# Performance work log

Hardware: AMD Instinct MI355X
Metric: run time of the kernel (lower is better)

The kernel has to match this reference:

```python
import jax, jax.numpy as jnp
import numpy as np

B, T, C, H = 4, 2048, 1024, 16
D = C // H  # key_dim = 64


def setup_inputs() -> dict:
    key = jax.random.key(0)
    k1, k2, k3 = jax.random.split(key, 3)
    x = jax.random.normal(k1, (B, T, C), dtype=jnp.float32)
    w_attn = jax.random.normal(k2, (C, 3 * C), dtype=jnp.float32) * 0.02
    b_attn = jnp.zeros((3 * C,), dtype=jnp.float32)
    w_proj = jax.random.normal(k3, (C, C), dtype=jnp.float32) * 0.02
    b_proj = jnp.zeros((C,), dtype=jnp.float32)
    return {"x": x, "w_attn": w_attn, "b_attn": b_attn,
            "w_proj": w_proj, "b_proj": b_proj}


def reference(x, w_attn, b_attn, w_proj, b_proj):
    b, t, c = x.shape
    d = c // H
    qkv = jnp.einsum('btc,cf->btf', x, w_attn) + b_attn  # [B,T,3C]
    q, k, v = jnp.split(qkv, 3, axis=-1)
    # [B,T,C] -> [B,H,T,D]
    q = q.reshape(b, t, H, d).transpose(0, 2, 1, 3)
    k = k.reshape(b, t, H, d).transpose(0, 2, 1, 3)
    v = v.reshape(b, t, H, d).transpose(0, 2, 1, 3)
    att = jnp.einsum('bhqd,bhkd->bhqk', q, k) / jnp.sqrt(jnp.float32(d))
    att = jax.nn.softmax(att, axis=-1)  # non-causal, full attention
    # dropout layers are identity at inference (rate=0.0 config)
    y = jnp.einsum('bhqk,bhkd->bhqd', att, v)
    y = y.transpose(0, 2, 1, 3).reshape(b, t, c)
    return jnp.einsum('btc,cf->btf', y, w_proj) + b_proj
```

## Files before the change

### kernel.cpp

```cpp
#include <hip/hip_runtime.h>
#include <math.h>

#define BB 4
#define TT 2048
#define CC 1024
#define HH 16
#define F3 3072
#define NTOK (BB*TT)
#define KDIM 1024

typedef __attribute__((ext_vector_type(8))) short short8;
typedef __attribute__((ext_vector_type(8))) unsigned short ushort8;
typedef __attribute__((ext_vector_type(8))) _Float16 half8;
typedef __attribute__((ext_vector_type(4))) unsigned short ushort4v;
typedef __attribute__((ext_vector_type(4))) float float4v;

static __device__ __forceinline__ unsigned short f2bf(float x) {
    union { float f; unsigned u; } v; v.f = x;
    unsigned r = v.u + 0x7fffu + ((v.u >> 16) & 1u);
    return (unsigned short)(r >> 16);
}
static __device__ __forceinline__ float bf2f(unsigned short h) {
    union { unsigned u; float f; } v; v.u = ((unsigned)h) << 16;
    return v.f;
}
static __device__ __forceinline__ unsigned short f2h(float x) {
    union { _Float16 h; unsigned short u; } v; v.h = (_Float16)x; return v.u;
}

static __device__ __forceinline__ void async16(const void* g, void* l) {
    __builtin_amdgcn_global_load_lds(
        (const __attribute__((address_space(1))) unsigned int*)g,
        (__attribute__((address_space(3))) unsigned int*)l, 16, 0, 0);
}

template <int C>
static __device__ __forceinline__ float dppf(float x) {
    return __int_as_float(
        __builtin_amdgcn_update_dpp(0, __float_as_int(x), C, 0xf, 0xf, true));
}
static __device__ __forceinline__ float red16_sum(float v) {
    v += dppf<0x128>(v);
    v += dppf<0x124>(v);
    v += dppf<0x4E>(v);
    v += dppf<0xB1>(v);
    return v;
}

#if __has_builtin(__builtin_amdgcn_exp2f)
#define EXP2(x) __builtin_amdgcn_exp2f(x)
#else
#define EXP2(x) __expf((x) * 0.6931471805599453f)
#endif

#define BAR()  asm volatile("s_barrier" ::: "memory")
#define VMW(n) asm volatile("s_waitcnt vmcnt(" #n ")" ::: "memory")

__global__ __launch_bounds__(256) void prep_w(
    const float* __restrict__ W, unsigned short* __restrict__ WtH,
    unsigned short* __restrict__ WtL, int N)
{
    __shared__ float Ls[64][65];
    const int t = threadIdx.x;
    const int n0 = blockIdx.x * 64, k0 = blockIdx.y * 64;
    const int cc = t & 63, rr = t >> 6;
    #pragma unroll
    for (int i = 0; i < 16; ++i) {
        const int row = rr + 4 * i;
        Ls[row][cc] = W[(long)(k0 + row) * N + n0 + cc];
    }
    __syncthreads();
    const int n = t >> 2, seg = (t & 3) << 4;
    ushort8 h0, h1, l0, l1;
    #pragma unroll
    for (int j = 0; j < 8; ++j) {
        float x0 = Ls[seg + j][n];
        h0[j] = f2bf(x0); l0[j] = f2bf(x0 - bf2f(h0[j]));
        float x1 = Ls[seg + 8 + j][n];
        h1[j] = f2bf(x1); l1[j] = f2bf(x1 - bf2f(h1[j]));
    }
    const long o = (long)(n0 + n) * KDIM + k0 + seg;
    *(ushort8*)(WtH + o) = h0;     *(ushort8*)(WtH + o + 8) = h1;
    *(ushort8*)(WtL + o) = l0;     *(ushort8*)(WtL + o + 8) = l1;
}

__global__ __launch_bounds__(256) void prep_w16(
    const float* __restrict__ W, unsigned short* __restrict__ WtF, int N)
{
    __shared__ float Ls[64][65];
    const int t = threadIdx.x;
    const int n0 = blockIdx.x * 64, k0 = blockIdx.y * 64;
    const int cc = t & 63, rr = t >> 6;
    #pragma unroll
    for (int i = 0; i < 16; ++i) {
        const int row = rr + 4 * i;
        Ls[row][cc] = W[(long)(k0 + row) * N + n0 + cc];
    }
    __syncthreads();
    const int n = t >> 2, seg = (t & 3) << 4;
    ushort8 h0, h1;
    #pragma unroll
    for (int j = 0; j < 8; ++j) {
        h0[j] = f2h(Ls[seg + j][n]);
        h1[j] = f2h(Ls[seg + 8 + j][n]);
    }
    const long o = (long)(n0 + n) * KDIM + k0 + seg;
    *(ushort8*)(WtF + o) = h0;     *(ushort8*)(WtF + o + 8) = h1;
}

__global__ __launch_bounds__(256) void split16(
    const float* __restrict__ X, unsigned short* __restrict__ XF)
{
    const long i = (long)blockIdx.x * 256 + threadIdx.x;
    const float4 v = ((const float4*)X)[i];
    ushort4v h;
    h[0] = f2h(v.x); h[1] = f2h(v.y); h[2] = f2h(v.z); h[3] = f2h(v.w);
    ((ushort4v*)XF)[i] = h;
}

__global__ __launch_bounds__(256) void gemm16_qkv(
    const unsigned short* __restrict__ A, const unsigned short* __restrict__ B,
    const float* __restrict__ bias, unsigned short* __restrict__ qkvp,
    unsigned short* __restrict__ VTp)
{
    __shared__ __align__(16) unsigned short sA[128 * 64];
    __shared__ __align__(16) unsigned short sB[128 * 64];

    const int tid = threadIdx.x;
    const int n0 = blockIdx.x * 128, m0 = blockIdx.y * 128;
    const int lane = tid & 63, w = tid >> 6;
    const int wm = w >> 1, wn = w & 1;
    const int l = lane & 15, quad = lane >> 4;

    unsigned short* const sbuf = (w < 2) ? sA : sB;
    const unsigned short* const gsrc = (w < 2) ? A + (long)m0 * KDIM
                                               : B + (long)n0 * KDIM;
    const int p128 = (w & 1) * 64 + lane;

    float4v acc[4][4];
    #pragma unroll
    for (int mt = 0; mt < 4; ++mt)
        #pragma unroll
        for (int nt = 0; nt < 4; ++nt)
            acc[mt][nt] = (float4v){0.f, 0.f, 0.f, 0.f};

    for (int k0 = 0; k0 < KDIM; k0 += 64) {
        #pragma unroll
        for (int i = 0; i < 8; ++i) {
            const int u = i * 128 + p128;
            const int r = u >> 3, ps = u & 7;
            const int s = (ps - r) & 7;
            async16(gsrc + (long)r * KDIM + k0 + s * 8, sbuf + u * 8);
        }
        __syncthreads();

        #pragma unroll
        for (int ks = 0; ks < 2; ++ks) {
            half8 fa[4];
            #pragma unroll
            for (int mt = 0; mt < 4; ++mt) {
                const int row = wm * 64 + mt * 16 + l;
                fa[mt] = *(const half8*)&sA[row * 64 + ((ks * 4 + quad + row) & 7) * 8];
            }
            #pragma unroll
            for (int nt = 0; nt < 4; ++nt) {
                const int row = wn * 64 + nt * 16 + l;
                const half8 fb = *(const half8*)&sB[row * 64 + ((ks * 4 + quad + row) & 7) * 8];
                #pragma unroll
                for (int mt = 0; mt < 4; ++mt)
                    acc[mt][nt] = __builtin_amdgcn_mfma_f32_16x16x32_f16(fa[mt], fb, acc[mt][nt], 0, 0, 0);
            }
        }
        __syncthreads();
    }

    #pragma unroll
    for (int nt = 0; nt < 4; ++nt) {
        const int col = n0 + wn * 64 + nt * 16 + l;
        const float bv = bias[col];
        if (col < 2048) {
            const float sc = (col < 1024) ? 0.18033688011112042f : 1.0f;
            #pragma unroll
            for (int mt = 0; mt < 4; ++mt)
                #pragma unroll
                for (int i = 0; i < 4; ++i) {
                    const long row = m0 + wm * 64 + mt * 16 + quad * 4 + i;
                    qkvp[row * F3 + col] = f2h((acc[mt][nt][i] + bv) * sc);
                }
        } else {
            const int d = col & 63;
            const int hh = (col >> 6) - 32;
            const int bb = m0 >> 11;
            const long vtoff = ((long)(bb * HH + hh) * 64 + d) * TT;
            #pragma unroll
            for (int mt = 0; mt < 4; ++mt) {
                const int t0 = (m0 & 2047) + wm * 64 + mt * 16 + quad * 4;
                ushort4v pk;
                #pragma unroll
                for (int i = 0; i < 4; ++i) pk[i] = f2bf(acc[mt][nt][i] + bv);
                *(ushort4v*)(VTp + vtoff + t0) = pk;
            }
        }
    }
}

__global__ __launch_bounds__(256) void gemm_split(
    const unsigned short* __restrict__ AH, const unsigned short* __restrict__ AL,
    const unsigned short* __restrict__ BH, const unsigned short* __restrict__ BL,
    const float* __restrict__ bias, void* __restrict__ outp,
    unsigned short* __restrict__ VTp, int N, int mode)
{
    __shared__ __align__(16) unsigned short sAH[128 * 32];
    __shared__ __align__(16) unsigned short sAL[128 * 32];
    __shared__ __align__(16) unsigned short sBH[128 * 32];
    __shared__ __align__(16) unsigned short sBL[128 * 32];

    const int tid = threadIdx.x;
    const int n0 = blockIdx.x * 128, m0 = blockIdx.y * 128;
    const int lane = tid & 63, w = tid >> 6;
    const int wm = w >> 1, wn = w & 1;
    const int l = lane & 15, quad = lane >> 4;

    unsigned short* const sbuf = (w == 0) ? sAH : (w == 1) ? sAL
                               : (w == 2) ? sBH : sBL;
    const unsigned short* const gsrc =
        (w == 0) ? AH + (long)m0 * KDIM : (w == 1) ? AL + (long)m0 * KDIM
      : (w == 2) ? BH + (long)n0 * KDIM : BL + (long)n0 * KDIM;
    const int lrow = lane >> 2;
    const int lseg = ((lane & 3) - (lane >> 3)) & 3;
    const unsigned short* const gbase = gsrc + (long)lrow * KDIM + lseg * 8;
    unsigned short* const lbase = sbuf + lane * 8;

    const int swz = ((quad + (l >> 1)) & 3) * 8;

    float4v acc[4][4];
    #pragma unroll
    for (int mt = 0; mt < 4; ++mt)
        #pragma unroll
        for (int nt = 0; nt < 4; ++nt)
            acc[mt][nt] = (float4v){0.f, 0.f, 0.f, 0.f};

    for (int k0 = 0; k0 < KDIM; k0 += 32) {
        #pragma unroll
        for (int i = 0; i < 8; ++i)
            async16(gbase + (long)i * 16 * KDIM + k0, lbase + i * 512);
        __syncthreads();

        short8 fah[4], fal[4];
        #pragma unroll
        for (int mt = 0; mt < 4; ++mt) {
            const int off = (wm * 64 + mt * 16 + l) * 32 + swz;
            fah[mt] = *(const short8*)&sAH[off];
            fal[mt] = *(const short8*)&sAL[off];
        }
        #pragma unroll
        for (int nt = 0; nt < 4; ++nt) {
            const int off = (wn * 64 + nt * 16 + l) * 32 + swz;
            const short8 fbh = *(const short8*)&sBH[off];
            const short8 fbl = *(const short8*)&sBL[off];
            #pragma unroll
            for (int mt = 0; mt < 4; ++mt) {
                acc[mt][nt] = __builtin_amdgcn_mfma_f32_16x16x32_bf16(fah[mt], fbh, acc[mt][nt], 0, 0, 0);
                acc[mt][nt] = __builtin_amdgcn_mfma_f32_16x16x32_bf16(fah[mt], fbl, acc[mt][nt], 0, 0, 0);
                acc[mt][nt] = __builtin_amdgcn_mfma_f32_16x16x32_bf16(fal[mt], fbh, acc[mt][nt], 0, 0, 0);
            }
        }
        __syncthreads();
    }

    #pragma unroll
    for (int nt = 0; nt < 4; ++nt) {
        const int col = n0 + wn * 64 + nt * 16 + l;
        const float bv = bias[col];
        #pragma unroll
        for (int mt = 0; mt < 4; ++mt)
            #pragma unroll
            for (int i = 0; i < 4; ++i) {
                const long row = m0 + wm * 64 + mt * 16 + quad * 4 + i;
                ((float*)outp)[row * N + col] = acc[mt][nt][i] + bv;
            }
    }
    (void)VTp; (void)mode;
}

#define STAGEKV(k0, bf) do { \
    async16(qkv + (base + (k0) + rK) * F3 + 1024 + hoff + sK * 8, &KV[bf][tid * 8]); \
    async16(VT + vtbase + (long)rK * TT + (k0) + sK * 8, &KV[2 + bf][tid * 8]); \
  } while (0)

#define ATTN_TILE(cur) do { \
    float4v sA[2][4]; \
    _Pragma("unroll") for (int qt = 0; qt < 2; ++qt) \
        _Pragma("unroll") for (int nt = 0; nt < 4; ++nt) \
            sA[qt][nt] = (float4v){0.f, 0.f, 0.f, 0.f}; \
     \
    __builtin_amdgcn_s_setprio(1); \
    _Pragma("unroll") for (int kit = 0; kit < 2; ++kit) { \
        const int seg = ((kit * 4 + quad) ^ xs) * 8; \
        _Pragma("unroll") for (int nt = 0; nt < 4; ++nt) { \
            const half8 kb = *(const half8*)&KV[cur][(16 * nt + l) * 64 + seg]; \
            sA[0][nt] = __builtin_amdgcn_mfma_f32_16x16x32_f16(qa[0][kit], kb, sA[0][nt], 0, 0, 0); \
            sA[1][nt] = __builtin_amdgcn_mfma_f32_16x16x32_f16(qa[1][kit], kb, sA[1][nt], 0, 0, 0); \
        } \
    } \
    __builtin_amdgcn_s_setprio(0); \
     \
    _Pragma("unroll") for (int qt = 0; qt < 2; ++qt) { \
        _Pragma("unroll") for (int nt = 0; nt < 4; ++nt) { \
            _Pragma("unroll") for (int i = 0; i < 4; ++i) { \
                const float p = EXP2(fminf(sA[qt][nt][i], 80.f)); \
                const unsigned pu = __float_as_uint(p); \
                l_part[qt][i] += __uint_as_float(pu & 0xFFFF0000u); \
                Ps[(wv * 32 + qt * 16 + quad * 4 + i) * 72 + 16 * nt + l] = \
                    (unsigned short)(pu >> 16); \
            } \
        } \
    } \
     \
    __builtin_amdgcn_s_setprio(1); \
    _Pragma("unroll") for (int kit = 0; kit < 2; ++kit) { \
        const short8 pa0 = *(const short8*)&Ps[(wv * 32 + l) * 72 + kit * 32 + quad * 8]; \
        const short8 pa1 = *(const short8*)&Ps[(wv * 32 + 16 + l) * 72 + kit * 32 + quad * 8]; \
        const int seg = ((kit * 4 + quad) ^ xs) * 8; \
        _Pragma("unroll") for (int dt = 0; dt < 4; ++dt) { \
            const short8 vb = *(const short8*)&KV[2 + cur][(16 * dt + l) * 64 + seg]; \
            acc[0][dt] = __builtin_amdgcn_mfma_f32_16x16x32_bf16(pa0, vb, acc[0][dt], 0, 0, 0); \
            acc[1][dt] = __builtin_amdgcn_mfma_f32_16x16x32_bf16(pa1, vb, acc[1][dt], 0, 0, 0); \
        } \
    } \
    __builtin_amdgcn_s_setprio(0); \
  } while (0)

__global__ __attribute__((amdgpu_flat_work_group_size(512, 512),
                          amdgpu_waves_per_eu(4)))
void attn_kernel(const unsigned short* __restrict__ qkv,
                 const unsigned short* __restrict__ VT,
                 unsigned short* __restrict__ yH,
                 unsigned short* __restrict__ yL)
{
    __shared__ __align__(16) unsigned short KV[4][64 * 64];
    __shared__ __align__(16) unsigned short Ps[256 * 72];

    const int tid = threadIdx.x;
    const int lid = blockIdx.x;
    const int work = (lid & 7) * 64 + (lid >> 3);
    const int q0 = (work & 7) * 256;
    const int bh = work >> 3;
    const int b = bh >> 4;
    const int hoff = (bh & 15) * 64;
    const long base = (long)(b * TT);
    const long vtbase = (long)bh * 64 * TT;

    const int lane = tid & 63;
    const int wv = tid >> 6;
    const int l = lane & 15;
    const int quad = lane >> 4;
    const int xs = l & 7;

    const int rK = tid >> 3;
    const int sK = (tid & 7) ^ (rK & 7);

    unsigned short* const KVf = &KV[0][0];

    #pragma unroll
    for (int i = 0; i < 4; ++i) {
        const int u = i * 512 + tid;
        const int r = u >> 3, s = (u & 7) ^ (r & 7);
        async16(qkv + (base + q0 + r) * F3 + hoff + s * 8, &KVf[u * 8]);
    }
    VMW(0); BAR();

    half8 qa[2][2];
    #pragma unroll
    for (int qt = 0; qt < 2; ++qt)
        #pragma unroll
        for (int kit = 0; kit < 2; ++kit) {
            const int seg = ((kit * 4 + quad) ^ xs) * 8;
            qa[qt][kit] = *(const half8*)&KVf[(wv * 32 + qt * 16 + l) * 64 + seg];
        }
    __syncthreads();

    float4v acc[2][4];
    float l_part[2][4];
    #pragma unroll
    for (int qt = 0; qt < 2; ++qt)
        #pragma unroll
        for (int dt = 0; dt < 4; ++dt) {
            acc[qt][dt] = (float4v){0.f, 0.f, 0.f, 0.f};
            l_part[qt][dt] = 0.f;
        }

    STAGEKV(0, 0);
    VMW(0); BAR();

    #pragma unroll 1
    for (int t = 0; t < TT / 64 - 1; ++t) {
        const int cur = t & 1;
        STAGEKV((t + 1) * 64, cur ^ 1);
        VMW(2);
        BAR();
        ATTN_TILE(cur);
        BAR();
    }
    VMW(0);
    BAR();
    ATTN_TILE(1);

    #pragma unroll
    for (int qt = 0; qt < 2; ++qt)
        #pragma unroll
        for (int i = 0; i < 4; ++i) {
            const float inv_l = 1.f / red16_sum(l_part[qt][i]);
            const long row = base + q0 + wv * 32 + qt * 16 + quad * 4 + i;
            #pragma unroll
            for (int dt = 0; dt < 4; ++dt) {
                const float o = acc[qt][dt][i] * inv_l;
                const unsigned short hh = f2bf(o);
                yH[row * CC + hoff + 16 * dt + l] = hh;
                yL[row * CC + hoff + 16 * dt + l] = f2bf(o - bf2f(hh));
            }
        }
}

extern "C" void kernel_launch(void* const* d_in, const int* in_sizes, int n_in,
                              void* d_out, int out_size, void* d_ws, size_t ws_size,
                              hipStream_t stream) {
    const float* x      = (const float*)d_in[0];
    const float* w_attn = (const float*)d_in[1];
    const float* b_attn = (const float*)d_in[2];
    const float* w_proj = (const float*)d_in[3];
    const float* b_proj = (const float*)d_in[4];
    float* out = (float*)d_out;

    char* wsb = (char*)d_ws;
    unsigned short* qkv = (unsigned short*)(wsb);
    unsigned short* VT  = (unsigned short*)(wsb + 50331648);
    unsigned short* xF  = (unsigned short*)(wsb + 67108864);
    unsigned short* yL  = (unsigned short*)(wsb + 83886080);
    unsigned short* WaF = (unsigned short*)(wsb + 100663296);
    unsigned short* WpH = (unsigned short*)(wsb + 106954752);
    unsigned short* WpL = (unsigned short*)(wsb + 109051904);

    prep_w16<<<dim3(F3 / 64, KDIM / 64), 256, 0, stream>>>(w_attn, WaF, F3);
    prep_w<<<dim3(CC / 64, KDIM / 64), 256, 0, stream>>>(w_proj, WpH, WpL, CC);
    split16<<<(NTOK * CC / 4) / 256, 256, 0, stream>>>(x, xF);

    gemm16_qkv<<<dim3(F3 / 128, NTOK / 128), 256, 0, stream>>>(
        xF, WaF, b_attn, qkv, VT);

    attn_kernel<<<dim3((TT / 256) * BB * HH), 512, 0, stream>>>(qkv, VT, xF, yL);

    gemm_split<<<dim3(CC / 128, NTOK / 128), 256, 0, stream>>>(
        xF, yL, WpH, WpL, b_proj, out, (unsigned short*)nullptr, CC, 0);
}
```

Before: 316.0 us.

## Compute softmax row sums via MFMA with ones vector and split P staging per q-tile

Replaces the per-element VALU accumulation of the softmax denominator (mask, add, then DPP cross-lane reduction) with an extra bf16 MFMA that multiplies the P tile by a ones vector, so row sums come out of the matrix unit already reduced. V fragments are now loaded into registers once per tile, and the P staging buffer is halved by processing the two 16-row query sub-tiles one after another, each writing and then consuming its own Ps slice. This trades VALU adds and DPP ops for extra MFMA issue and more live vector registers, and it shrinks LDS use. The sub-tile ordering relies on Ps reuse within a wave without an explicit barrier, which assumes in-order LDS access within the wave.

```diff
diff --git a/kernel.cpp b/kernel.cpp
--- a/kernel.cpp
+++ b/kernel.cpp
@@ -32,19 +32,6 @@
     __builtin_amdgcn_global_load_lds(
         (const __attribute__((address_space(1))) unsigned int*)g,
         (__attribute__((address_space(3))) unsigned int*)l, 16, 0, 0);
-}
-
-template <int C>
-static __device__ __forceinline__ float dppf(float x) {
-    return __int_as_float(
-        __builtin_amdgcn_update_dpp(0, __float_as_int(x), C, 0xf, 0xf, true));
-}
-static __device__ __forceinline__ float red16_sum(float v) {
-    v += dppf<0x128>(v);
-    v += dppf<0x124>(v);
-    v += dppf<0x4E>(v);
-    v += dppf<0xB1>(v);
-    return v;
 }
 
 #if __has_builtin(__builtin_amdgcn_exp2f)
@@ -305,30 +292,30 @@
     } \
     __builtin_amdgcn_s_setprio(0); \
      \
+    short8 vb[2][4]; \
+    _Pragma("unroll") for (int kit = 0; kit < 2; ++kit) { \
+        const int seg = ((kit * 4 + quad) ^ xs) * 8; \
+        _Pragma("unroll") for (int dt = 0; dt < 4; ++dt) \
+            vb[kit][dt] = *(const short8*)&KV[2 + cur][(16 * dt + l) * 64 + seg]; \
+    } \
+     \
     _Pragma("unroll") for (int qt = 0; qt < 2; ++qt) { \
         _Pragma("unroll") for (int nt = 0; nt < 4; ++nt) { \
             _Pragma("unroll") for (int i = 0; i < 4; ++i) { \
                 const float p = EXP2(fminf(sA[qt][nt][i], 80.f)); \
-                const unsigned pu = __float_as_uint(p); \
-                l_part[qt][i] += __uint_as_float(pu & 0xFFFF0000u); \
-                Ps[(wv * 32 + qt * 16 + quad * 4 + i) * 72 + 16 * nt + l] = \
-                    (unsigned short)(pu >> 16); \
+                Ps[(wv * 16 + quad * 4 + i) * 72 + 16 * nt + l] = \
+                    (unsigned short)(__float_as_uint(p) >> 16); \
             } \
         } \
+        __builtin_amdgcn_s_setprio(1); \
+        _Pragma("unroll") for (int kit = 0; kit < 2; ++kit) { \
+            const short8 pa = *(const short8*)&Ps[(wv * 16 + l) * 72 + kit * 32 + quad * 8]; \
+            acc_l[qt] = __builtin_amdgcn_mfma_f32_16x16x32_bf16(pa, ones, acc_l[qt], 0, 0, 0); \
+            _Pragma("unroll") for (int dt = 0; dt < 4; ++dt) \
+                acc[qt][dt] = __builtin_amdgcn_mfma_f32_16x16x32_bf16(pa, vb[kit][dt], acc[qt][dt], 0, 0, 0); \
+        } \
+        __builtin_amdgcn_s_setprio(0); \
     } \
-     \
-    __builtin_amdgcn_s_setprio(1); \
-    _Pragma("unroll") for (int kit = 0; kit < 2; ++kit) { \
-        const short8 pa0 = *(const short8*)&Ps[(wv * 32 + l) * 72 + kit * 32 + quad * 8]; \
-        const short8 pa1 = *(const short8*)&Ps[(wv * 32 + 16 + l) * 72 + kit * 32 + quad * 8]; \
-        const int seg = ((kit * 4 + quad) ^ xs) * 8; \
-        _Pragma("unroll") for (int dt = 0; dt < 4; ++dt) { \
-            const short8 vb = *(const short8*)&KV[2 + cur][(16 * dt + l) * 64 + seg]; \
-            acc[0][dt] = __builtin_amdgcn_mfma_f32_16x16x32_bf16(pa0, vb, acc[0][dt], 0, 0, 0); \
-            acc[1][dt] = __builtin_amdgcn_mfma_f32_16x16x32_bf16(pa1, vb, acc[1][dt], 0, 0, 0); \
-        } \
-    } \
-    __builtin_amdgcn_s_setprio(0); \
   } while (0)
 
 __global__ __attribute__((amdgpu_flat_work_group_size(512, 512),
@@ -339,7 +326,7 @@
                  unsigned short* __restrict__ yL)
 {
     __shared__ __align__(16) unsigned short KV[4][64 * 64];
-    __shared__ __align__(16) unsigned short Ps[256 * 72];
+    __shared__ __align__(16) unsigned short Ps[128 * 72];
 
     const int tid = threadIdx.x;
     const int lid = blockIdx.x;
@@ -362,6 +349,9 @@
 
     unsigned short* const KVf = &KV[0][0];
 
+    const short8 ones = {0x3F80, 0x3F80, 0x3F80, 0x3F80,
+                         0x3F80, 0x3F80, 0x3F80, 0x3F80};
+
     #pragma unroll
     for (int i = 0; i < 4; ++i) {
         const int u = i * 512 + tid;
@@ -381,14 +371,14 @@
     __syncthreads();
 
     float4v acc[2][4];
-    float l_part[2][4];
-    #pragma unroll
-    for (int qt = 0; qt < 2; ++qt)
-        #pragma unroll
-        for (int dt = 0; dt < 4; ++dt) {
+    float4v acc_l[2];
+    #pragma unroll
+    for (int qt = 0; qt < 2; ++qt) {
+        acc_l[qt] = (float4v){0.f, 0.f, 0.f, 0.f};
+        #pragma unroll
+        for (int dt = 0; dt < 4; ++dt)
             acc[qt][dt] = (float4v){0.f, 0.f, 0.f, 0.f};
-            l_part[qt][dt] = 0.f;
-        }
+    }
 
     STAGEKV(0, 0);
     VMW(0); BAR();
@@ -410,7 +400,7 @@
     for (int qt = 0; qt < 2; ++qt)
         #pragma unroll
         for (int i = 0; i < 4; ++i) {
-            const float inv_l = 1.f / red16_sum(l_part[qt][i]);
+            const float inv_l = 1.f / acc_l[qt][i];
             const long row = base + q0 + wv * 32 + qt * 16 + quad * 4 + i;
             #pragma unroll
             for (int dt = 0; dt < 4; ++dt) {
```

New measurement: 328.8 us. 4.1% more time.
